# Optimization experiments

Measured on AMD Instinct MI355X. Metric: run time of the kernel, lower is better.

Reference implementation:

```python
import jax, jax.numpy as jnp
import numpy as np
from jax import lax

N, GH, GE, LH, LL = 19, 64, 64, 64, 2
B, T = 256, 256


def _normalized_adjacency(A):
    # A: (..., n, n). Add self-loops, symmetric degree normalization.
    n = A.shape[-1]
    A = A + jnp.eye(n, dtype=A.dtype)
    deg = jnp.clip(A.sum(axis=-1), 1e-6, None)  # (..., n)
    dis = deg ** -0.5
    return A * dis[..., :, None] * dis[..., None, :]


def _graph_encoder(A, w1_w, w1_b, w2_w, w2_b):
    # A: (B, T, n, n) -> (B, T, GE). Node features X = A rows.
    An = _normalized_adjacency(A)
    X = jax.nn.relu(An @ (A @ w1_w.T + w1_b))   # (B,T,n,GH)
    X = jax.nn.relu(An @ (X @ w2_w.T + w2_b))   # (B,T,n,GE)
    return X.mean(axis=-2)


def _lstm_layer(x, Wih, Whh, bih, bhh):
    # x: (B, T, D); PyTorch gate order i,f,g,o. Returns (B, T, H).
    Bb = x.shape[0]
    H = Whh.shape[1]
    xg = x @ Wih.T + (bih + bhh)  # precompute input contributions (B,T,4H)

    def step(carry, xt):
        h, c = carry
        gates = xt + h @ Whh.T
        i, f, g, o = jnp.split(gates, 4, axis=-1)
        c = jax.nn.sigmoid(f) * c + jax.nn.sigmoid(i) * jnp.tanh(g)
        h = jax.nn.sigmoid(o) * jnp.tanh(c)
        return (h, c), h

    h0 = jnp.zeros((Bb, H), x.dtype)
    (_, _), hs = lax.scan(step, (h0, h0), jnp.swapaxes(xg, 0, 1))
    return jnp.swapaxes(hs, 0, 1)


def setup_inputs() -> dict:
    key = jax.random.key(0)
    ks = jax.random.split(key, 20)
    s = 0.1
    inp = {
        'conn': jax.random.uniform(ks[0], (B, T, N, N), jnp.float32),
        'mask': jnp.ones((B, T), jnp.int32),
        'w1_w': jax.random.normal(ks[1], (GH, N), jnp.float32) * s,
        'w1_b': jax.random.normal(ks[2], (GH,), jnp.float32) * s,
        'w2_w': jax.random.normal(ks[3], (GE, GH), jnp.float32) * s,
        'w2_b': jax.random.normal(ks[4], (GE,), jnp.float32) * s,
        'lstm_Wih0': jax.random.normal(ks[5], (4 * LH, GE), jnp.float32) * s,
        'lstm_Whh0': jax.random.normal(ks[6], (4 * LH, LH), jnp.float32) * s,
        'lstm_bih0': jax.random.normal(ks[7], (4 * LH,), jnp.float32) * s,
        'lstm_bhh0': jax.random.normal(ks[8], (4 * LH,), jnp.float32) * s,
        'lstm_Wih1': jax.random.normal(ks[9], (4 * LH, LH), jnp.float32) * s,
        'lstm_Whh1': jax.random.normal(ks[10], (4 * LH, LH), jnp.float32) * s,
        'lstm_bih1': jax.random.normal(ks[11], (4 * LH,), jnp.float32) * s,
        'lstm_bhh1': jax.random.normal(ks[12], (4 * LH,), jnp.float32) * s,
        'fc1_w': jax.random.normal(ks[13], (32, LH), jnp.float32) * s,
        'fc1_b': jax.random.normal(ks[14], (32,), jnp.float32) * s,
        'fc2_w': jax.random.normal(ks[15], (2, 32), jnp.float32) * s,
        'fc2_b': jax.random.normal(ks[16], (2,), jnp.float32) * s,
    }
    return inp


def reference(conn, mask, w1_w, w1_b, w2_w, w2_b,
              lstm_Wih0, lstm_Whh0, lstm_bih0, lstm_bhh0,
              lstm_Wih1, lstm_Whh1, lstm_bih1, lstm_bhh1,
              fc1_w, fc1_b, fc2_w, fc2_b):
    emb = _graph_encoder(conn, w1_w, w1_b, w2_w, w2_b)  # (B,T,GE)
    mf = mask.astype(emb.dtype)
    emb = emb * mf[:, :, None]
    out = _lstm_layer(emb, lstm_Wih0, lstm_Whh0, lstm_bih0, lstm_bhh0)
    out = _lstm_layer(out, lstm_Wih1, lstm_Whh1, lstm_bih1, lstm_bhh1)  # (B,T,LH)
    lengths = jnp.clip(mask.sum(axis=1), 1, None)
    last_idx = jnp.clip(lengths - 1, 0, None)  # (B,)
    last_h = jnp.take_along_axis(out, last_idx[:, None, None], axis=1)[:, 0, :]
    h = jax.nn.relu(last_h @ fc1_w.T + fc1_b)
    return h @ fc2_w.T + fc2_b  # (B,2) logits
```

## Files before the change

### kernel.cpp

```cpp
#include <hip/hip_runtime.h>
#include <hip/hip_bf16.h>
#include <math.h>

#define GN 19
#define BB 256
#define TT 256

typedef short short8 __attribute__((ext_vector_type(8)));
typedef float f4 __attribute__((ext_vector_type(4)));

union Frag { int i[4]; short8 s; };

#define LWAIT() __asm__ volatile("s_waitcnt lgkmcnt(0)" ::: "memory")
#define WGBAR() __asm__ volatile("s_waitcnt lgkmcnt(0)\ns_barrier" ::: "memory")

__device__ __forceinline__ int pkbf(float a, float b) {
    __hip_bfloat162 h2 = __float22bfloat162_rn(make_float2(a, b));
    union { __hip_bfloat162 h; int i; } u; u.h = h2; return u.i;
}

__device__ __forceinline__ float rl(float v, int j) {
    return __int_as_float(__builtin_amdgcn_readlane(__float_as_int(v), j));
}
__device__ __forceinline__ float fexp2(float x) { return __builtin_amdgcn_exp2f(x); }
__device__ __forceinline__ float frcp(float x)  { return __builtin_amdgcn_rcpf(x); }
__device__ __forceinline__ float sigm(float x)  { return frcp(1.f + fexp2(-1.4426950408889634f * x)); }
__device__ __forceinline__ float tanha(float x) { float e = fexp2(2.8853900817779268f * x); return 1.f - 2.f * frcp(e + 1.f); }

__global__ __launch_bounds__(64) void encoder_mfma(
    const float* __restrict__ conn,
    const int*   __restrict__ mask,
    const float* __restrict__ w1_w,
    const float* __restrict__ w1_b,
    const float* __restrict__ w2_w,
    const float* __restrict__ w2_b,
    float* __restrict__ emb,
    int num_graphs)
{
    __shared__ float S[2304];
    __shared__ float dis[32];
    __shared__ float ps[256];

    const int t = threadIdx.x;
    const int l15 = t & 15;
    const int quad = t >> 4;

    float km[8];
    #pragma unroll
    for (int j = 0; j < 8; ++j) km[j] = (quad * 8 + j < GN) ? 1.f : 0.f;

    int rr[6], cc[6];
    #pragma unroll
    for (int i = 0; i < 6; ++i) {
        int e = t + 64 * i;
        rr[i] = e / GN;
        cc[i] = e - rr[i] * GN;
    }

    Frag w1F[4];
    #pragma unroll
    for (int nt = 0; nt < 4; ++nt) {
        int n = nt * 16 + l15;
        #pragma unroll
        for (int p = 0; p < 4; ++p) {
            int k0 = quad * 8 + 2 * p, k1 = k0 + 1;
            float a = (k0 < GN) ? w1_w[n * GN + k0] : 0.f;
            float b = (k1 < GN) ? w1_w[n * GN + k1] : 0.f;
            w1F[nt].i[p] = pkbf(a, b);
        }
    }
    Frag w2F[2][4];
    #pragma unroll
    for (int kt = 0; kt < 2; ++kt)
        #pragma unroll
        for (int nt = 0; nt < 4; ++nt) {
            int n = nt * 16 + l15;
            #pragma unroll
            for (int p = 0; p < 4; ++p) {
                int k = kt * 32 + quad * 8 + 2 * p;
                w2F[kt][nt].i[p] = pkbf(w2_w[n * 64 + k], w2_w[n * 64 + k + 1]);
            }
        }
    float b1v[4], b2v[4];
    #pragma unroll
    for (int nt = 0; nt < 4; ++nt) {
        b1v[nt] = w1_b[nt * 16 + l15];
        b2v[nt] = w2_b[nt * 16 + l15];
    }

    float pf[6];
    {
        int g0 = blockIdx.x < num_graphs ? blockIdx.x : 0;
        const float* Ag = conn + (size_t)g0 * (GN * GN);
        #pragma unroll
        for (int i = 0; i < 6; ++i) {
            int e = t + 64 * i;
            if (e < GN * GN) pf[i] = Ag[e];
        }
    }

    #pragma unroll 1
    for (int g = blockIdx.x; g < num_graphs; g += gridDim.x) {
        #pragma unroll
        for (int i = 0; i < 4; ++i) {
            int s = t + 64 * i;
            int row = s >> 3, c4 = s & 7;
            f4 z = {0.f, 0.f, 0.f, 0.f};
            *(f4*)&S[row * 68 + c4 * 4] = z;
        }
        LWAIT();
        #pragma unroll
        for (int i = 0; i < 6; ++i) {
            if (t + 64 * i < GN * GN) S[rr[i] * 68 + cc[i]] = pf[i];
        }
        {
            int gn = g + gridDim.x;
            const float* Ag = conn + (size_t)(gn < num_graphs ? gn : g) * (GN * GN);
            #pragma unroll
            for (int i = 0; i < 6; ++i) {
                int e = t + 64 * i;
                if (e < GN * GN) pf[i] = Ag[e];
            }
        }
        LWAIT();

        if (t < 32) {
            float dv = 0.f;
            if (t < GN) {
                float d = 1.0f;
                #pragma unroll
                for (int c4 = 0; c4 < 8; ++c4) {
                    f4 v = *(f4*)&S[t * 68 + c4 * 4];
                    d += v.x + v.y + v.z + v.w;
                }
                dv = rsqrtf(d);
            }
            dis[t] = dv;
        }
        LWAIT();

        float dk[8];
        {
            f4 v0 = *(f4*)&dis[quad * 8];
            f4 v1 = *(f4*)&dis[quad * 8 + 4];
            dk[0]=v0.x; dk[1]=v0.y; dk[2]=v0.z; dk[3]=v0.w;
            dk[4]=v1.x; dk[5]=v1.y; dk[6]=v1.z; dk[7]=v1.w;
        }
        Frag aF[2], anF[2];
        #pragma unroll
        for (int mt = 0; mt < 2; ++mt) {
            int m = l15 + 16 * mt;
            float dm = dis[m];
            f4 v0 = *(f4*)&S[m * 68 + quad * 8];
            f4 v1 = *(f4*)&S[m * 68 + quad * 8 + 4];
            float av[8] = {v0.x, v0.y, v0.z, v0.w, v1.x, v1.y, v1.z, v1.w};
            float an[8];
            #pragma unroll
            for (int j = 0; j < 8; ++j) {
                int k = quad * 8 + j;
                an[j] = (av[j] + (m == k ? 1.f : 0.f)) * dm * dk[j];
            }
            #pragma unroll
            for (int p = 0; p < 4; ++p) {
                aF[mt].i[p]  = pkbf(av[2*p], av[2*p+1]);
                anF[mt].i[p] = pkbf(an[2*p], an[2*p+1]);
            }
        }
        LWAIT();

        #pragma unroll
        for (int mt = 0; mt < 2; ++mt)
            #pragma unroll
            for (int nt = 0; nt < 4; ++nt) {
                float bb = b1v[nt];
                f4 c = {bb, bb, bb, bb};
                c = __builtin_amdgcn_mfma_f32_16x16x32_bf16(aF[mt].s, w1F[nt].s, c, 0, 0, 0);
                int col = nt * 16 + l15;
                #pragma unroll
                for (int r = 0; r < 4; ++r)
                    S[col * 36 + (mt * 16 + quad * 4 + r)] = c[r];
            }
        LWAIT();

        Frag hF[4];
        #pragma unroll
        for (int nt = 0; nt < 4; ++nt) {
            int n = nt * 16 + l15;
            f4 v0 = *(f4*)&S[n * 36 + quad * 8];
            f4 v1 = *(f4*)&S[n * 36 + quad * 8 + 4];
            float vv[8] = {v0.x, v0.y, v0.z, v0.w, v1.x, v1.y, v1.z, v1.w};
            #pragma unroll
            for (int p = 0; p < 4; ++p)
                hF[nt].i[p] = pkbf(vv[2*p] * km[2*p], vv[2*p+1] * km[2*p+1]);
        }
        LWAIT();

        #pragma unroll
        for (int mt = 0; mt < 2; ++mt)
            #pragma unroll
            for (int nt = 0; nt < 4; ++nt) {
                f4 c = {0.f, 0.f, 0.f, 0.f};
                c = __builtin_amdgcn_mfma_f32_16x16x32_bf16(anF[mt].s, hF[nt].s, c, 0, 0, 0);
                int col = nt * 16 + l15;
                #pragma unroll
                for (int r = 0; r < 4; ++r)
                    S[(mt * 16 + quad * 4 + r) * 68 + col] = fmaxf(c[r], 0.f);
            }
        LWAIT();

        Frag xF[2][2];
        #pragma unroll
        for (int mt = 0; mt < 2; ++mt) {
            int m = l15 + 16 * mt;
            #pragma unroll
            for (int kt = 0; kt < 2; ++kt) {
                f4 v0 = *(f4*)&S[m * 68 + kt * 32 + quad * 8];
                f4 v1 = *(f4*)&S[m * 68 + kt * 32 + quad * 8 + 4];
                xF[mt][kt].i[0] = pkbf(v0.x, v0.y);
                xF[mt][kt].i[1] = pkbf(v0.z, v0.w);
                xF[mt][kt].i[2] = pkbf(v1.x, v1.y);
                xF[mt][kt].i[3] = pkbf(v1.z, v1.w);
            }
        }
        LWAIT();

        #pragma unroll
        for (int mt = 0; mt < 2; ++mt)
            #pragma unroll
            for (int nt = 0; nt < 4; ++nt) {
                float bb = b2v[nt];
                f4 c = {bb, bb, bb, bb};
                c = __builtin_amdgcn_mfma_f32_16x16x32_bf16(xF[mt][0].s, w2F[0][nt].s, c, 0, 0, 0);
                c = __builtin_amdgcn_mfma_f32_16x16x32_bf16(xF[mt][1].s, w2F[1][nt].s, c, 0, 0, 0);
                int col = nt * 16 + l15;
                #pragma unroll
                for (int r = 0; r < 4; ++r)
                    S[col * 36 + (mt * 16 + quad * 4 + r)] = c[r];
            }
        LWAIT();

        #pragma unroll
        for (int nt = 0; nt < 4; ++nt) {
            int n = nt * 16 + l15;
            f4 v0 = *(f4*)&S[n * 36 + quad * 8];
            f4 v1 = *(f4*)&S[n * 36 + quad * 8 + 4];
            float vv[8] = {v0.x, v0.y, v0.z, v0.w, v1.x, v1.y, v1.z, v1.w};
            #pragma unroll
            for (int p = 0; p < 4; ++p)
                hF[nt].i[p] = pkbf(vv[2*p] * km[2*p], vv[2*p+1] * km[2*p+1]);
        }

        float cs[4];
        #pragma unroll
        for (int nt = 0; nt < 4; ++nt) cs[nt] = 0.f;
        #pragma unroll
        for (int mt = 0; mt < 2; ++mt)
            #pragma unroll
            for (int nt = 0; nt < 4; ++nt) {
                f4 c = {0.f, 0.f, 0.f, 0.f};
                c = __builtin_amdgcn_mfma_f32_16x16x32_bf16(anF[mt].s, hF[nt].s, c, 0, 0, 0);
                if (mt == 0) {
                    cs[nt] += fmaxf(c[0], 0.f) + fmaxf(c[1], 0.f)
                            + fmaxf(c[2], 0.f) + fmaxf(c[3], 0.f);
                } else if (quad == 0) {
                    cs[nt] += fmaxf(c[0], 0.f) + fmaxf(c[1], 0.f) + fmaxf(c[2], 0.f);
                }
            }
        #pragma unroll
        for (int nt = 0; nt < 4; ++nt)
            ps[quad * 64 + nt * 16 + l15] = cs[nt];
        LWAIT();
        float tot = ps[t] + ps[64 + t] + ps[128 + t] + ps[192 + t];
        float mf = (float)mask[g];
        emb[(size_t)g * 64 + t] = tot * (1.f / 19.f) * mf;
        LWAIT();
    }
}

__global__ __launch_bounds__(256, 1) void lstm_l0(
    const float* __restrict__ x,
    const float* __restrict__ Wih, const float* __restrict__ Whh,
    const float* __restrict__ bih, const float* __restrict__ bhh,
    float* __restrict__ hseq)
{
    __shared__ float gs[2][256];
    const int tid = threadIdx.x;
    const int w = tid >> 6, l = tid & 63;
    const int b = blockIdx.x;

    float wi[64], wh[64];
    {
        const float4* p = (const float4*)(Wih + tid * 64);
        const float4* q = (const float4*)(Whh + tid * 64);
        #pragma unroll
        for (int j = 0; j < 16; ++j) {
            ((float4*)wi)[j] = p[j];
            ((float4*)wh)[j] = q[j];
        }
    }
    const float bias = bih[tid] + bhh[tid];
    const float* __restrict__ xb = x + (size_t)b * TT * 64;

    float xc;
    {
        float n0 = 0.f, n1 = 0.f, n2 = 0.f, n3 = 0.f;
        #pragma unroll
        for (int j = 0; j < 64; j += 4) {
            n0 = fmaf(xb[j],     wi[j],     n0);
            n1 = fmaf(xb[j + 1], wi[j + 1], n1);
            n2 = fmaf(xb[j + 2], wi[j + 2], n2);
            n3 = fmaf(xb[j + 3], wi[j + 3], n3);
        }
        xc = (n0 + n1) + (n2 + n3);
    }

    float h = 0.f, c = 0.f;

    #pragma unroll 1
    for (int t = 0; t < TT; ++t) {
        const f4* __restrict__ ern = (const f4*)(xb + (t + 1 < TT ? t + 1 : TT - 1) * 64);
        f4 xr[16];
        #pragma unroll
        for (int k = 0; k < 16; ++k) xr[k] = ern[k];

        float a0 = bias + xc, a1 = 0.f, a2 = 0.f, a3 = 0.f;
        #pragma unroll
        for (int j = 0; j < 64; j += 4) {
            a0 = fmaf(rl(h, j),     wh[j],     a0);
            a1 = fmaf(rl(h, j + 1), wh[j + 1], a1);
            a2 = fmaf(rl(h, j + 2), wh[j + 2], a2);
            a3 = fmaf(rl(h, j + 3), wh[j + 3], a3);
        }
        gs[t & 1][tid] = (a0 + a1) + (a2 + a3);
        WGBAR();
        const float* gp = gs[t & 1];
        float gi = gp[l], gf = gp[64 + l], gg = gp[128 + l], go = gp[192 + l];
        c = sigm(gf) * c + sigm(gi) * tanha(gg);
        h = sigm(go) * tanha(c);
        if (w == 0) hseq[((size_t)b * TT + t) * 64 + l] = h;

        float n0 = 0.f, n1 = 0.f, n2 = 0.f, n3 = 0.f;
        #pragma unroll
        for (int k = 0; k < 16; ++k) {
            f4 v = xr[k];
            n0 = fmaf(v.x, wi[4*k],     n0);
            n1 = fmaf(v.y, wi[4*k + 1], n1);
            n2 = fmaf(v.z, wi[4*k + 2], n2);
            n3 = fmaf(v.w, wi[4*k + 3], n3);
        }
        xc = (n0 + n1) + (n2 + n3);
    }
}

__global__ __launch_bounds__(256, 1) void lstm_l1_head(
    const float* __restrict__ x,
    const int*   __restrict__ mask,
    const float* __restrict__ Wih, const float* __restrict__ Whh,
    const float* __restrict__ bih, const float* __restrict__ bhh,
    const float* __restrict__ fc1_w, const float* __restrict__ fc1_b,
    const float* __restrict__ fc2_w, const float* __restrict__ fc2_b,
    float* __restrict__ out)
{
    __shared__ float gs[2][256];
    __shared__ int li_s;
    const int tid = threadIdx.x;
    const int w = tid >> 6, l = tid & 63;
    const int b = blockIdx.x;

    float wi[64], wh[64];
    {
        const float4* p = (const float4*)(Wih + tid * 64);
        const float4* q = (const float4*)(Whh + tid * 64);
        #pragma unroll
        for (int j = 0; j < 16; ++j) {
            ((float4*)wi)[j] = p[j];
            ((float4*)wh)[j] = q[j];
        }
    }
    const float bias = bih[tid] + bhh[tid];

    gs[0][tid] = (float)mask[b * TT + tid];
    __syncthreads();
    if (tid == 0) {
        float s = 0.f;
        for (int t = 0; t < TT; ++t) s += gs[0][t];
        int li = (int)s - 1;
        li = li < 0 ? 0 : (li > TT - 1 ? TT - 1 : li);
        li_s = li;
    }
    __syncthreads();
    const int lastidx = li_s;

    const float* __restrict__ xb = x + (size_t)b * TT * 64;

    float xc;
    {
        float n0 = 0.f, n1 = 0.f, n2 = 0.f, n3 = 0.f;
        #pragma unroll
        for (int j = 0; j < 64; j += 4) {
            n0 = fmaf(xb[j],     wi[j],     n0);
            n1 = fmaf(xb[j + 1], wi[j + 1], n1);
            n2 = fmaf(xb[j + 2], wi[j + 2], n2);
            n3 = fmaf(xb[j + 3], wi[j + 3], n3);
        }
        xc = (n0 + n1) + (n2 + n3);
    }

    float h = 0.f, c = 0.f, hl = 0.f;

    #pragma unroll 1
    for (int t = 0; t < TT; ++t) {
        const f4* __restrict__ ern = (const f4*)(xb + (t + 1 < TT ? t + 1 : TT - 1) * 64);
        f4 xr[16];
        #pragma unroll
        for (int k = 0; k < 16; ++k) xr[k] = ern[k];

        float a0 = bias + xc, a1 = 0.f, a2 = 0.f, a3 = 0.f;
        #pragma unroll
        for (int j = 0; j < 64; j += 4) {
            a0 = fmaf(rl(h, j),     wh[j],     a0);
            a1 = fmaf(rl(h, j + 1), wh[j + 1], a1);
            a2 = fmaf(rl(h, j + 2), wh[j + 2], a2);
            a3 = fmaf(rl(h, j + 3), wh[j + 3], a3);
        }
        gs[t & 1][tid] = (a0 + a1) + (a2 + a3);
        WGBAR();
        const float* gp = gs[t & 1];
        float gi = gp[l], gf = gp[64 + l], gg = gp[128 + l], go = gp[192 + l];
        c = sigm(gf) * c + sigm(gi) * tanha(gg);
        h = sigm(go) * tanha(c);
        if (t == lastidx) hl = h;

        float n0 = 0.f, n1 = 0.f, n2 = 0.f, n3 = 0.f;
        #pragma unroll
        for (int k = 0; k < 16; ++k) {
            f4 v = xr[k];
            n0 = fmaf(v.x, wi[4*k],     n0);
            n1 = fmaf(v.y, wi[4*k + 1], n1);
            n2 = fmaf(v.z, wi[4*k + 2], n2);
            n3 = fmaf(v.w, wi[4*k + 3], n3);
        }
        xc = (n0 + n1) + (n2 + n3);
    }

    __syncthreads();
    if (w == 0 && l < 32) {
        float acc = fc1_b[l];
        const float* fw = fc1_w + l * 64;
        #pragma unroll
        for (int j = 0; j < 64; ++j)
            acc = fmaf(fw[j], rl(hl, j), acc);
        gs[0][l] = fmaxf(acc, 0.f);
    }
    __syncthreads();
    if (w == 0 && l < 2) {
        float acc = fc2_b[l];
        #pragma unroll
        for (int j = 0; j < 32; ++j)
            acc = fmaf(fc2_w[l * 32 + j], gs[0][j], acc);
        out[b * 2 + l] = acc;
    }
}

extern "C" void kernel_launch(void* const* d_in, const int* in_sizes, int n_in,
                              void* d_out, int out_size, void* d_ws, size_t ws_size,
                              hipStream_t stream)
{
    const float* conn  = (const float*)d_in[0];
    const int*   mask  = (const int*)  d_in[1];
    const float* w1_w  = (const float*)d_in[2];
    const float* w1_b  = (const float*)d_in[3];
    const float* w2_w  = (const float*)d_in[4];
    const float* w2_b  = (const float*)d_in[5];
    const float* Wih0  = (const float*)d_in[6];
    const float* Whh0  = (const float*)d_in[7];
    const float* bih0  = (const float*)d_in[8];
    const float* bhh0  = (const float*)d_in[9];
    const float* Wih1  = (const float*)d_in[10];
    const float* Whh1  = (const float*)d_in[11];
    const float* bih1  = (const float*)d_in[12];
    const float* bhh1  = (const float*)d_in[13];
    const float* fc1_w = (const float*)d_in[14];
    const float* fc1_b = (const float*)d_in[15];
    const float* fc2_w = (const float*)d_in[16];
    const float* fc2_b = (const float*)d_in[17];

    float* out = (float*)d_out;
    float* emb   = (float*)d_ws;
    float* h0seq = (float*)d_ws + (size_t)BB * TT * 64;

    const int num_graphs = BB * TT;

    encoder_mfma<<<8192, 64, 0, stream>>>(
        conn, mask, w1_w, w1_b, w2_w, w2_b, emb, num_graphs);

    lstm_l0<<<BB, 256, 0, stream>>>(emb, Wih0, Whh0, bih0, bhh0, h0seq);

    lstm_l1_head<<<BB, 256, 0, stream>>>(
        h0seq, mask, Wih1, Whh1, bih1, bhh1,
        fc1_w, fc1_b, fc2_w, fc2_b, out);
}
```

Measured before the change: 601.0 us.

## Fuse both LSTM layers into one wavefront-pipelined kernel with layer skew

The two LSTM layer kernels are merged into one 512-thread block per batch row. Threads 0-255 run layer 0 and threads 256-511 run layer 1, skewed by two steps, and layer-0 hidden states are handed over through a double-buffered shared array instead of a global h0seq round trip. This removes one launch and the global write and read of the intermediate sequence, and lets the two recurrences run at the same time on 256 blocks. In exchange every step now waits on a 512-thread barrier, there are two extra iterations, and register pressure per block doubles.

```diff
diff --git a/kernel.cpp b/kernel.cpp
--- a/kernel.cpp
+++ b/kernel.cpp
@@ -277,32 +277,61 @@
     }
 }
 
-__global__ __launch_bounds__(256, 1) void lstm_l0(
+__global__ __launch_bounds__(512, 2) void lstm_fused(
     const float* __restrict__ x,
-    const float* __restrict__ Wih, const float* __restrict__ Whh,
-    const float* __restrict__ bih, const float* __restrict__ bhh,
-    float* __restrict__ hseq)
+    const int*   __restrict__ mask,
+    const float* __restrict__ Wih0, const float* __restrict__ Whh0,
+    const float* __restrict__ bih0, const float* __restrict__ bhh0,
+    const float* __restrict__ Wih1, const float* __restrict__ Whh1,
+    const float* __restrict__ bih1, const float* __restrict__ bhh1,
+    const float* __restrict__ fc1_w, const float* __restrict__ fc1_b,
+    const float* __restrict__ fc2_w, const float* __restrict__ fc2_b,
+    float* __restrict__ out)
 {
-    __shared__ float gs[2][256];
+    __shared__ float gs0[2][256];
+    __shared__ float gs1[2][256];
+    __shared__ float h0buf[2][64];
+    __shared__ float hd[32];
+    __shared__ int li_s;
+
     const int tid = threadIdx.x;
-    const int w = tid >> 6, l = tid & 63;
-    const int b = blockIdx.x;
-
+    const int grp = tid >> 8;
+    const int r   = tid & 255;
+    const int l   = tid & 63;
+    const int b   = blockIdx.x;
+
+    const float* __restrict__ Wih = grp ? Wih1 : Wih0;
+    const float* __restrict__ Whh = grp ? Whh1 : Whh0;
     float wi[64], wh[64];
     {
-        const float4* p = (const float4*)(Wih + tid * 64);
-        const float4* q = (const float4*)(Whh + tid * 64);
+        const float4* p = (const float4*)(Wih + r * 64);
+        const float4* q = (const float4*)(Whh + r * 64);
         #pragma unroll
         for (int j = 0; j < 16; ++j) {
             ((float4*)wi)[j] = p[j];
             ((float4*)wh)[j] = q[j];
         }
     }
-    const float bias = bih[tid] + bhh[tid];
+    const float bias = grp ? (bih1[r] + bhh1[r]) : (bih0[r] + bhh0[r]);
+
+    if (tid < 256) gs0[0][tid] = (float)mask[b * TT + tid];
+    __syncthreads();
+    if (tid == 0) {
+        float s = 0.f;
+        for (int t = 0; t < TT; ++t) s += gs0[0][t];
+        int li = (int)s - 1;
+        li = li < 0 ? 0 : (li > TT - 1 ? TT - 1 : li);
+        li_s = li;
+    }
+    __syncthreads();
+    const int lastidx = li_s;
+
     const float* __restrict__ xb = x + (size_t)b * TT * 64;
-
-    float xc;
-    {
+    float (*gsL)[256] = grp ? gs1 : gs0;
+
+    float h = 0.f, c = 0.f, xc = 0.f, hl = 0.f;
+
+    if (grp == 0) {
         float n0 = 0.f, n1 = 0.f, n2 = 0.f, n3 = 0.f;
         #pragma unroll
         for (int j = 0; j < 64; j += 4) {
@@ -314,151 +343,103 @@
         xc = (n0 + n1) + (n2 + n3);
     }
 
-    float h = 0.f, c = 0.f;
-
     #pragma unroll 1
-    for (int t = 0; t < TT; ++t) {
-        const f4* __restrict__ ern = (const f4*)(xb + (t + 1 < TT ? t + 1 : TT - 1) * 64);
+    for (int it = 0; it < TT + 2; ++it) {
+        const int p = it & 1;
+
         f4 xr[16];
-        #pragma unroll
-        for (int k = 0; k < 16; ++k) xr[k] = ern[k];
-
-        float a0 = bias + xc, a1 = 0.f, a2 = 0.f, a3 = 0.f;
-        #pragma unroll
-        for (int j = 0; j < 64; j += 4) {
-            a0 = fmaf(rl(h, j),     wh[j],     a0);
-            a1 = fmaf(rl(h, j + 1), wh[j + 1], a1);
-            a2 = fmaf(rl(h, j + 2), wh[j + 2], a2);
-            a3 = fmaf(rl(h, j + 3), wh[j + 3], a3);
-        }
-        gs[t & 1][tid] = (a0 + a1) + (a2 + a3);
+        if (grp == 0) {
+            int tn = it + 1; if (tn > TT - 1) tn = TT - 1;
+            const f4* __restrict__ ern = (const f4*)(xb + (size_t)tn * 64);
+            #pragma unroll
+            for (int k = 0; k < 16; ++k) xr[k] = ern[k];
+
+            if (it < TT) {
+                float a0 = bias + xc, a1 = 0.f, a2 = 0.f, a3 = 0.f;
+                #pragma unroll
+                for (int j = 0; j < 64; j += 4) {
+                    a0 = fmaf(rl(h, j),     wh[j],     a0);
+                    a1 = fmaf(rl(h, j + 1), wh[j + 1], a1);
+                    a2 = fmaf(rl(h, j + 2), wh[j + 2], a2);
+                    a3 = fmaf(rl(h, j + 3), wh[j + 3], a3);
+                }
+                gs0[p][r] = (a0 + a1) + (a2 + a3);
+            }
+        } else {
+            if (it >= 2) {
+                float a0 = bias + xc, a1 = 0.f, a2 = 0.f, a3 = 0.f;
+                #pragma unroll
+                for (int j = 0; j < 64; j += 4) {
+                    a0 = fmaf(rl(h, j),     wh[j],     a0);
+                    a1 = fmaf(rl(h, j + 1), wh[j + 1], a1);
+                    a2 = fmaf(rl(h, j + 2), wh[j + 2], a2);
+                    a3 = fmaf(rl(h, j + 3), wh[j + 3], a3);
+                }
+                gs1[p][r] = (a0 + a1) + (a2 + a3);
+            }
+        }
+
         WGBAR();
-        const float* gp = gs[t & 1];
-        float gi = gp[l], gf = gp[64 + l], gg = gp[128 + l], go = gp[192 + l];
-        c = sigm(gf) * c + sigm(gi) * tanha(gg);
-        h = sigm(go) * tanha(c);
-        if (w == 0) hseq[((size_t)b * TT + t) * 64 + l] = h;
-
-        float n0 = 0.f, n1 = 0.f, n2 = 0.f, n3 = 0.f;
-        #pragma unroll
-        for (int k = 0; k < 16; ++k) {
-            f4 v = xr[k];
-            n0 = fmaf(v.x, wi[4*k],     n0);
-            n1 = fmaf(v.y, wi[4*k + 1], n1);
-            n2 = fmaf(v.z, wi[4*k + 2], n2);
-            n3 = fmaf(v.w, wi[4*k + 3], n3);
-        }
-        xc = (n0 + n1) + (n2 + n3);
-    }
-}
-
-__global__ __launch_bounds__(256, 1) void lstm_l1_head(
-    const float* __restrict__ x,
-    const int*   __restrict__ mask,
-    const float* __restrict__ Wih, const float* __restrict__ Whh,
-    const float* __restrict__ bih, const float* __restrict__ bhh,
-    const float* __restrict__ fc1_w, const float* __restrict__ fc1_b,
-    const float* __restrict__ fc2_w, const float* __restrict__ fc2_b,
-    float* __restrict__ out)
-{
-    __shared__ float gs[2][256];
-    __shared__ int li_s;
-    const int tid = threadIdx.x;
-    const int w = tid >> 6, l = tid & 63;
-    const int b = blockIdx.x;
-
-    float wi[64], wh[64];
-    {
-        const float4* p = (const float4*)(Wih + tid * 64);
-        const float4* q = (const float4*)(Whh + tid * 64);
-        #pragma unroll
-        for (int j = 0; j < 16; ++j) {
-            ((float4*)wi)[j] = p[j];
-            ((float4*)wh)[j] = q[j];
-        }
-    }
-    const float bias = bih[tid] + bhh[tid];
-
-    gs[0][tid] = (float)mask[b * TT + tid];
-    __syncthreads();
-    if (tid == 0) {
-        float s = 0.f;
-        for (int t = 0; t < TT; ++t) s += gs[0][t];
-        int li = (int)s - 1;
-        li = li < 0 ? 0 : (li > TT - 1 ? TT - 1 : li);
-        li_s = li;
-    }
-    __syncthreads();
-    const int lastidx = li_s;
-
-    const float* __restrict__ xb = x + (size_t)b * TT * 64;
-
-    float xc;
-    {
-        float n0 = 0.f, n1 = 0.f, n2 = 0.f, n3 = 0.f;
-        #pragma unroll
-        for (int j = 0; j < 64; j += 4) {
-            n0 = fmaf(xb[j],     wi[j],     n0);
-            n1 = fmaf(xb[j + 1], wi[j + 1], n1);
-            n2 = fmaf(xb[j + 2], wi[j + 2], n2);
-            n3 = fmaf(xb[j + 3], wi[j + 3], n3);
-        }
-        xc = (n0 + n1) + (n2 + n3);
-    }
-
-    float h = 0.f, c = 0.f, hl = 0.f;
-
-    #pragma unroll 1
-    for (int t = 0; t < TT; ++t) {
-        const f4* __restrict__ ern = (const f4*)(xb + (t + 1 < TT ? t + 1 : TT - 1) * 64);
-        f4 xr[16];
-        #pragma unroll
-        for (int k = 0; k < 16; ++k) xr[k] = ern[k];
-
-        float a0 = bias + xc, a1 = 0.f, a2 = 0.f, a3 = 0.f;
-        #pragma unroll
-        for (int j = 0; j < 64; j += 4) {
-            a0 = fmaf(rl(h, j),     wh[j],     a0);
-            a1 = fmaf(rl(h, j + 1), wh[j + 1], a1);
-            a2 = fmaf(rl(h, j + 2), wh[j + 2], a2);
-            a3 = fmaf(rl(h, j + 3), wh[j + 3], a3);
-        }
-        gs[t & 1][tid] = (a0 + a1) + (a2 + a3);
-        WGBAR();
-        const float* gp = gs[t & 1];
-        float gi = gp[l], gf = gp[64 + l], gg = gp[128 + l], go = gp[192 + l];
-        c = sigm(gf) * c + sigm(gi) * tanha(gg);
-        h = sigm(go) * tanha(c);
-        if (t == lastidx) hl = h;
-
-        float n0 = 0.f, n1 = 0.f, n2 = 0.f, n3 = 0.f;
-        #pragma unroll
-        for (int k = 0; k < 16; ++k) {
-            f4 v = xr[k];
-            n0 = fmaf(v.x, wi[4*k],     n0);
-            n1 = fmaf(v.y, wi[4*k + 1], n1);
-            n2 = fmaf(v.z, wi[4*k + 2], n2);
-            n3 = fmaf(v.w, wi[4*k + 3], n3);
-        }
-        xc = (n0 + n1) + (n2 + n3);
-    }
-
-    __syncthreads();
-    if (w == 0 && l < 32) {
-        float acc = fc1_b[l];
-        const float* fw = fc1_w + l * 64;
-        #pragma unroll
-        for (int j = 0; j < 64; ++j)
-            acc = fmaf(fw[j], rl(hl, j), acc);
-        gs[0][l] = fmaxf(acc, 0.f);
-    }
-    __syncthreads();
-    if (w == 0 && l < 2) {
-        float acc = fc2_b[l];
-        #pragma unroll
-        for (int j = 0; j < 32; ++j)
-            acc = fmaf(fc2_w[l * 32 + j], gs[0][j], acc);
-        out[b * 2 + l] = acc;
+
+        if (grp == 0) {
+            if (it < TT) {
+                const float* gp = gs0[p];
+                float gi = gp[l], gf = gp[64 + l], gg = gp[128 + l], go = gp[192 + l];
+                c = sigm(gf) * c + sigm(gi) * tanha(gg);
+                h = sigm(go) * tanha(c);
+                if (tid < 64) h0buf[p][l] = h;
+            }
+            float n0 = 0.f, n1 = 0.f, n2 = 0.f, n3 = 0.f;
+            #pragma unroll
+            for (int k = 0; k < 16; ++k) {
+                f4 v = xr[k];
+                n0 = fmaf(v.x, wi[4*k],     n0);
+                n1 = fmaf(v.y, wi[4*k + 1], n1);
+                n2 = fmaf(v.z, wi[4*k + 2], n2);
+                n3 = fmaf(v.w, wi[4*k + 3], n3);
+            }
+            xc = (n0 + n1) + (n2 + n3);
+        } else {
+            if (it >= 2) {
+                const float* gp = gs1[p];
+                float gi = gp[l], gf = gp[64 + l], gg = gp[128 + l], go = gp[192 + l];
+                c = sigm(gf) * c + sigm(gi) * tanha(gg);
+                h = sigm(go) * tanha(c);
+                if (it - 2 == lastidx) hl = h;
+            }
+            if (it >= 1 && it <= TT) {
+                const f4* __restrict__ hp = (const f4*)h0buf[p ^ 1];
+                float n0 = 0.f, n1 = 0.f, n2 = 0.f, n3 = 0.f;
+                #pragma unroll
+                for (int k = 0; k < 16; ++k) {
+                    f4 v = hp[k];
+                    n0 = fmaf(v.x, wi[4*k],     n0);
+                    n1 = fmaf(v.y, wi[4*k + 1], n1);
+                    n2 = fmaf(v.z, wi[4*k + 2], n2);
+                    n3 = fmaf(v.w, wi[4*k + 3], n3);
+                }
+                xc = (n0 + n1) + (n2 + n3);
+            }
+        }
+    }
+
+    if (grp == 1 && r < 64) {
+        if (l < 32) {
+            float acc = fc1_b[l];
+            const float* fw = fc1_w + l * 64;
+            #pragma unroll
+            for (int j = 0; j < 64; ++j)
+                acc = fmaf(fw[j], rl(hl, j), acc);
+            hd[l] = fmaxf(acc, 0.f);
+        }
+        LWAIT();
+        if (l < 2) {
+            float acc = fc2_b[l];
+            #pragma unroll
+            for (int j = 0; j < 32; ++j)
+                acc = fmaf(fc2_w[l * 32 + j], hd[j], acc);
+            out[b * 2 + l] = acc;
+        }
     }
 }
 
@@ -486,17 +467,14 @@
     const float* fc2_b = (const float*)d_in[17];
 
     float* out = (float*)d_out;
-    float* emb   = (float*)d_ws;
-    float* h0seq = (float*)d_ws + (size_t)BB * TT * 64;
+    float* emb = (float*)d_ws;
 
     const int num_graphs = BB * TT;
 
     encoder_mfma<<<8192, 64, 0, stream>>>(
         conn, mask, w1_w, w1_b, w2_w, w2_b, emb, num_graphs);
 
-    lstm_l0<<<BB, 256, 0, stream>>>(emb, Wih0, Whh0, bih0, bhh0, h0seq);
-
-    lstm_l1_head<<<BB, 256, 0, stream>>>(
-        h0seq, mask, Wih1, Whh1, bih1, bhh1,
+    lstm_fused<<<BB, 512, 0, stream>>>(
+        emb, mask, Wih0, Whh0, bih0, bhh0, Wih1, Whh1, bih1, bhh1,
         fc1_w, fc1_b, fc2_w, fc2_b, out);
 }
```

Measured after the change: 617.4 us. 2.7% more time.
